# Kernel tuning notes

Hardware: AMD Instinct MI355X
Metric: run time of the kernel (lower is better)

The kernel has to match this reference:

```python
import jax, jax.numpy as jnp
import numpy as np
from jax import lax

B, T, K = 32, 2048, 1024


def setup_inputs() -> dict:
    key = jax.random.key(0)
    x = jax.random.normal(key, (B, T, K), dtype=jnp.float32)
    return {"x": x}


def reference(x) -> jnp.ndarray:
    # x: [B, T, K]. Max-plus DP:
    #   out[:, 0]   = x[:, 0]
    #   out[:, i+1] = x[:, i+1] + max(out[:, i], shift_right(out[:, i], -inf))
    neg_inf = jnp.asarray(-jnp.inf, dtype=x.dtype)
    x_t = jnp.swapaxes(x, 0, 1)  # [T, B, K] time-major for scan

    def step(carry, xi):
        # carry: [B, K] = out row i; xi: [B, K] = x row i+1
        shifted = jnp.concatenate(
            [jnp.full_like(carry[:, :1], neg_inf), carry[:, :-1]], axis=1
        )
        new = xi + jnp.maximum(carry, shifted)
        return new, new

    init = x_t[0]
    _, rows = lax.scan(step, init, x_t[1:])  # rows: [T-1, B, K]
    out = jnp.concatenate([init[None], rows], axis=0)  # [T, B, K]
    return jnp.swapaxes(out, 0, 1)  # [B, T, K]
```

## Files before the change

### kernel.cpp

```cpp
#include <hip/hip_runtime.h>
#include <math.h>


#define BB 32
#define TT 2048
#define KK 1024
#define NG 4
#define NW 4
#define WW 64
#define GW (NW * WW)
#define RR 32
#define NT (TT / RR)
#define NSTEP (NT + NW - 1)

__global__ __launch_bounds__(256, 1)
void harddtw_hyb(const float* __restrict__ x, float* __restrict__ out,
                 int* __restrict__ flags, float* __restrict__ bws)
{
    const int bid  = blockIdx.x;
    const int g    = bid & (NG - 1);
    const int b    = bid >> 2;
    const int w    = threadIdx.x >> 6;
    const int lane = threadIdx.x & 63;
    const bool lz  = (lane == 0);
    const bool l16 = (lane == 16), l32 = (lane == 32), l48 = (lane == 48);

    const int kc = g * GW + w * WW + lane;
    const size_t base = (size_t)b * TT * KK;
    const float* xl  = x + base + kc;
    float*       olb = out + base + kc;

    int* myflag = flags + bid;
    int* upflag = flags + bid - 1;
    float*       mybw = bws + (size_t)bid * TT;
    const float* upbw = bws + (size_t)(bid - 1) * TT;

    __shared__ float bnd[NW - 1][2][RR];

    float pv = 0.0f;
    float left_prev = 0.0f;
    float corner = 0.0f;
    float bcur = -INFINITY;
    unsigned long long bp[16];
#pragma unroll
    for (int i = 0; i < 16; ++i) bp[i] = 0ull;

    const bool wpub = (w == NW - 1) && (g < NG - 1);

#pragma unroll 1
    for (int s = 0; s < NSTEP; ++s) {
        const int r = s - w;
        if (r >= 0 && r < NT) {
            const float* gp = xl + (size_t)r * RR * KK;
            float td[RR];
#pragma unroll
            for (int j = 0; j < RR; ++j)
                td[j] = gp[(size_t)j * KK];
            __builtin_amdgcn_sched_barrier(0);

            if (w == 0) {
                if (g > 0) {
                    while (__hip_atomic_load(upflag, __ATOMIC_RELAXED,
                                             __HIP_MEMORY_SCOPE_AGENT) < r + 1)
                        __builtin_amdgcn_s_sleep(1);
                    __asm__ volatile("" ::: "memory");
                    if (r == 0) {
                        if (lz) bcur = 0.0f;
                        else if (lane < RR)
                            bcur = __hip_atomic_load(upbw + lane - 1,
                                       __ATOMIC_RELAXED, __HIP_MEMORY_SCOPE_AGENT);
                    } else {
                        if (lane < RR)
                            bcur = __hip_atomic_load(
                                       upbw + (size_t)r * RR + lane - 1,
                                       __ATOMIC_RELAXED, __HIP_MEMORY_SCOPE_AGENT);
                    }
                }
            } else {
                float e = (lane >= 1 && lane < RR) ? bnd[w - 1][r & 1][lane - 1]
                                                   : 0.0f;
                bcur = lz ? corner : e;
                corner = bnd[w - 1][r & 1][RR - 1];
            }

            float* ol = olb + (size_t)r * RR * KK;
            float bpe = 0.0f;
#pragma unroll
            for (int j = 0; j < RR; ++j) {
                float xv = td[j];
                float bv = __int_as_float(
                    __builtin_amdgcn_readlane(__float_as_int(bcur), j));
                float left = lz ? bv : left_prev;
                float n = xv + fmaxf(pv, left);

                int ni = __float_as_int(n);
                int di = __builtin_amdgcn_update_dpp(ni, ni, 0x111, 0xf, 0xf,
                                                     false);
                float sh = __int_as_float(di);
                float v15 = __int_as_float(__builtin_amdgcn_readlane(ni, 15));
                float v31 = __int_as_float(__builtin_amdgcn_readlane(ni, 31));
                float v47 = __int_as_float(__builtin_amdgcn_readlane(ni, 47));
                if (l16) sh = v15;
                if (l32) sh = v31;
                if (l48) sh = v47;

                *ol = n;
                ol += KK;

                if (w < NW - 1) {
                    if (lane == 63) bnd[w][r & 1][j] = n;
                } else {
                    if ((j & 1) == 0) {
                        bpe = n;
                    } else {
                        union { float f[2]; unsigned long long u; } cv;
                        cv.f[0] = bpe; cv.f[1] = n;
                        bp[j >> 1] = cv.u;
                    }
                }

                pv = n; left_prev = sh;
            }

            if (wpub) {
                if (lane == 63) {
                    unsigned long long* bwp =
                        (unsigned long long*)(mybw + (size_t)r * RR);
#pragma unroll
                    for (int i = 0; i < 16; ++i)
                        __hip_atomic_store(bwp + i, bp[i], __ATOMIC_RELAXED,
                                           __HIP_MEMORY_SCOPE_AGENT);
                }
                __asm__ volatile("s_waitcnt vmcnt(0)" ::: "memory");
                if (lz)
                    __hip_atomic_store(myflag, r + 1, __ATOMIC_RELAXED,
                                       __HIP_MEMORY_SCOPE_AGENT);
            }
        }
        __syncthreads();
    }
}

extern "C" void kernel_launch(void* const* d_in, const int* in_sizes, int n_in,
                              void* d_out, int out_size, void* d_ws, size_t ws_size,
                              hipStream_t stream) {
    (void)in_sizes; (void)n_in; (void)out_size; (void)ws_size;
    const float* x = (const float*)d_in[0];
    float* out = (float*)d_out;
    int* flags = (int*)d_ws;
    float* bws = (float*)((char*)d_ws + 4096);

    (void)hipMemsetAsync(flags, 0, BB * NG * sizeof(int), stream);

    harddtw_hyb<<<dim3(BB * NG), dim3(NW * 64), 0, stream>>>(x, out, flags, bws);
}
```

Before: 630.4 us.

## Give each wavefront its own batch row and chain column groups via global flags

Restructures the work split. Each block's four wavefronts now handle four different batch rows, and each block covers one 64-column slice, giving 16 column groups per batch. This drops the intra-block wavefront pipeline that used shared memory and a barrier every step. Column groups instead hand off boundaries through global flags and workspace per wavefront. The intent is to remove the per-step __syncthreads and the pipeline fill and drain skew. The cost is a longer cross-block dependency chain (16 groups instead of 4 per batch), more global flag polling, and more workspace traffic.

```diff
diff --git a/kernel.cpp b/kernel.cpp
--- a/kernel.cpp
+++ b/kernel.cpp
@@ -5,139 +5,121 @@
 #define BB 32
 #define TT 2048
 #define KK 1024
-#define NG 4
-#define NW 4
+#define NG 16
+#define NWB 4
 #define WW 64
-#define GW (NW * WW)
 #define RR 32
 #define NT (TT / RR)
-#define NSTEP (NT + NW - 1)
 
 __global__ __launch_bounds__(256, 1)
-void harddtw_hyb(const float* __restrict__ x, float* __restrict__ out,
+void harddtw_tlp(const float* __restrict__ x, float* __restrict__ out,
                  int* __restrict__ flags, float* __restrict__ bws)
 {
     const int bid  = blockIdx.x;
     const int g    = bid & (NG - 1);
-    const int b    = bid >> 2;
+    const int bc   = bid >> 4;
     const int w    = threadIdx.x >> 6;
     const int lane = threadIdx.x & 63;
     const bool lz  = (lane == 0);
     const bool l16 = (lane == 16), l32 = (lane == 32), l48 = (lane == 48);
 
-    const int kc = g * GW + w * WW + lane;
+    const int b  = bc * NWB + w;
+    const int kc = g * WW + lane;
     const size_t base = (size_t)b * TT * KK;
     const float* xl  = x + base + kc;
     float*       olb = out + base + kc;
 
-    int* myflag = flags + bid;
-    int* upflag = flags + bid - 1;
-    float*       mybw = bws + (size_t)bid * TT;
-    const float* upbw = bws + (size_t)(bid - 1) * TT;
+    const int fidx = (b << 4) | g;
+    int* myflag = flags + fidx;
+    int* upflag = myflag - 1;
+    float*       mybw = bws + (size_t)fidx * TT;
+    const float* upbw = mybw - TT;
 
-    __shared__ float bnd[NW - 1][2][RR];
+    const bool pub = (g < NG - 1);
 
     float pv = 0.0f;
     float left_prev = 0.0f;
-    float corner = 0.0f;
-    float bcur = -INFINITY;
     unsigned long long bp[16];
 #pragma unroll
     for (int i = 0; i < 16; ++i) bp[i] = 0ull;
 
-    const bool wpub = (w == NW - 1) && (g < NG - 1);
+#pragma unroll 1
+    for (int r = 0; r < NT; ++r) {
+        const float* gp = xl + (size_t)r * RR * KK;
+        float td[RR];
+#pragma unroll
+        for (int j = 0; j < RR; ++j)
+            td[j] = gp[(size_t)j * KK];
+        __builtin_amdgcn_sched_barrier(0);
 
-#pragma unroll 1
-    for (int s = 0; s < NSTEP; ++s) {
-        const int r = s - w;
-        if (r >= 0 && r < NT) {
-            const float* gp = xl + (size_t)r * RR * KK;
-            float td[RR];
+        float bcur = -INFINITY;
+        if (g > 0) {
+            while (__hip_atomic_load(upflag, __ATOMIC_RELAXED,
+                                     __HIP_MEMORY_SCOPE_AGENT) < r + 1)
+                __builtin_amdgcn_s_sleep(1);
+            __asm__ volatile("" ::: "memory");
+            if (r == 0) {
+                if (lz) bcur = 0.0f;
+                else if (lane < RR)
+                    bcur = __hip_atomic_load(upbw + lane - 1,
+                               __ATOMIC_RELAXED, __HIP_MEMORY_SCOPE_AGENT);
+            } else {
+                if (lane < RR)
+                    bcur = __hip_atomic_load(
+                               upbw + (size_t)r * RR + lane - 1,
+                               __ATOMIC_RELAXED, __HIP_MEMORY_SCOPE_AGENT);
+            }
+        }
+
+        float* ol = olb + (size_t)r * RR * KK;
+        float bpe = 0.0f;
 #pragma unroll
-            for (int j = 0; j < RR; ++j)
-                td[j] = gp[(size_t)j * KK];
-            __builtin_amdgcn_sched_barrier(0);
+        for (int j = 0; j < RR; ++j) {
+            float xv = td[j];
+            float bv = __int_as_float(
+                __builtin_amdgcn_readlane(__float_as_int(bcur), j));
+            float left = lz ? bv : left_prev;
+            float n = xv + fmaxf(pv, left);
 
-            if (w == 0) {
-                if (g > 0) {
-                    while (__hip_atomic_load(upflag, __ATOMIC_RELAXED,
-                                             __HIP_MEMORY_SCOPE_AGENT) < r + 1)
-                        __builtin_amdgcn_s_sleep(1);
-                    __asm__ volatile("" ::: "memory");
-                    if (r == 0) {
-                        if (lz) bcur = 0.0f;
-                        else if (lane < RR)
-                            bcur = __hip_atomic_load(upbw + lane - 1,
-                                       __ATOMIC_RELAXED, __HIP_MEMORY_SCOPE_AGENT);
-                    } else {
-                        if (lane < RR)
-                            bcur = __hip_atomic_load(
-                                       upbw + (size_t)r * RR + lane - 1,
-                                       __ATOMIC_RELAXED, __HIP_MEMORY_SCOPE_AGENT);
-                    }
-                }
+            int ni = __float_as_int(n);
+            int di = __builtin_amdgcn_update_dpp(ni, ni, 0x111, 0xf, 0xf,
+                                                 false);
+            float sh = __int_as_float(di);
+            float v15 = __int_as_float(__builtin_amdgcn_readlane(ni, 15));
+            float v31 = __int_as_float(__builtin_amdgcn_readlane(ni, 31));
+            float v47 = __int_as_float(__builtin_amdgcn_readlane(ni, 47));
+            if (l16) sh = v15;
+            if (l32) sh = v31;
+            if (l48) sh = v47;
+
+            *ol = n;
+            ol += KK;
+
+            if ((j & 1) == 0) {
+                bpe = n;
             } else {
-                float e = (lane >= 1 && lane < RR) ? bnd[w - 1][r & 1][lane - 1]
-                                                   : 0.0f;
-                bcur = lz ? corner : e;
-                corner = bnd[w - 1][r & 1][RR - 1];
+                union { float f[2]; unsigned long long u; } cv;
+                cv.f[0] = bpe; cv.f[1] = n;
+                bp[j >> 1] = cv.u;
             }
 
-            float* ol = olb + (size_t)r * RR * KK;
-            float bpe = 0.0f;
+            pv = n; left_prev = sh;
+        }
+
+        if (pub) {
+            if (lane == 63) {
+                unsigned long long* bwp =
+                    (unsigned long long*)(mybw + (size_t)r * RR);
 #pragma unroll
-            for (int j = 0; j < RR; ++j) {
-                float xv = td[j];
-                float bv = __int_as_float(
-                    __builtin_amdgcn_readlane(__float_as_int(bcur), j));
-                float left = lz ? bv : left_prev;
-                float n = xv + fmaxf(pv, left);
-
-                int ni = __float_as_int(n);
-                int di = __builtin_amdgcn_update_dpp(ni, ni, 0x111, 0xf, 0xf,
-                                                     false);
-                float sh = __int_as_float(di);
-                float v15 = __int_as_float(__builtin_amdgcn_readlane(ni, 15));
-                float v31 = __int_as_float(__builtin_amdgcn_readlane(ni, 31));
-                float v47 = __int_as_float(__builtin_amdgcn_readlane(ni, 47));
-                if (l16) sh = v15;
-                if (l32) sh = v31;
-                if (l48) sh = v47;
-
-                *ol = n;
-                ol += KK;
-
-                if (w < NW - 1) {
-                    if (lane == 63) bnd[w][r & 1][j] = n;
-                } else {
-                    if ((j & 1) == 0) {
-                        bpe = n;
-                    } else {
-                        union { float f[2]; unsigned long long u; } cv;
-                        cv.f[0] = bpe; cv.f[1] = n;
-                        bp[j >> 1] = cv.u;
-                    }
-                }
-
-                pv = n; left_prev = sh;
-            }
-
-            if (wpub) {
-                if (lane == 63) {
-                    unsigned long long* bwp =
-                        (unsigned long long*)(mybw + (size_t)r * RR);
-#pragma unroll
-                    for (int i = 0; i < 16; ++i)
-                        __hip_atomic_store(bwp + i, bp[i], __ATOMIC_RELAXED,
-                                           __HIP_MEMORY_SCOPE_AGENT);
-                }
-                __asm__ volatile("s_waitcnt vmcnt(0)" ::: "memory");
-                if (lz)
-                    __hip_atomic_store(myflag, r + 1, __ATOMIC_RELAXED,
+                for (int i = 0; i < 16; ++i)
+                    __hip_atomic_store(bwp + i, bp[i], __ATOMIC_RELAXED,
                                        __HIP_MEMORY_SCOPE_AGENT);
             }
+            __asm__ volatile("s_waitcnt vmcnt(0)" ::: "memory");
+            if (lz)
+                __hip_atomic_store(myflag, r + 1, __ATOMIC_RELAXED,
+                                   __HIP_MEMORY_SCOPE_AGENT);
         }
-        __syncthreads();
     }
 }
 
@@ -152,5 +134,6 @@
 
     (void)hipMemsetAsync(flags, 0, BB * NG * sizeof(int), stream);
 
-    harddtw_hyb<<<dim3(BB * NG), dim3(NW * 64), 0, stream>>>(x, out, flags, bws);
+    harddtw_tlp<<<dim3((BB / NWB) * NG), dim3(NWB * 64), 0, stream>>>(
+        x, out, flags, bws);
 }
```

Result: no change. 629.6 us (-0.1%).
